# Kernel tuning notes

Hardware: AMD Instinct MI355X
Metric: run time of the kernel (lower is better)

## Reference

```python
import jax, jax.numpy as jnp
import numpy as np

N = 50000      # nodes
E = 1600000    # edges (avg degree 32)
F_IN = 128
HID = 256
C = 40


def setup_inputs() -> dict:
    key = jax.random.key(0)
    ks = jax.random.split(key, 12)
    x = jax.random.normal(ks[0], (N, F_IN), jnp.float32)
    edge_index = jax.random.randint(ks[1], (2, E), 0, N, dtype=jnp.int32)

    def glorot(k, fan_in, fan_out):
        s = jnp.sqrt(2.0 / (fan_in + fan_out)).astype(jnp.float32)
        return jax.random.normal(k, (fan_in, fan_out), jnp.float32) * s

    return {
        "x": x,
        "edge_index": edge_index,
        "W1": glorot(ks[2], F_IN, HID), "b1": jnp.zeros((HID,), jnp.float32),
        "W2": glorot(ks[3], HID, HID),  "b2": jnp.zeros((HID,), jnp.float32),
        "W3": glorot(ks[4], HID, HID),  "b3": jnp.zeros((HID,), jnp.float32),
        "W4": glorot(ks[5], HID, C),    "b4": jnp.zeros((C,), jnp.float32),
    }


def _gcn_conv(x, W, b, src, dst, norm_e, self_norm):
    # PyG GCNConv: h = X W; out_j = sum_i norm_ij * h_i  (+ self-loop term) + b
    h = x @ W                                   # [N, F_out]
    msg = h[src] * norm_e[:, None]              # [E, F_out] gather + scale
    agg = jax.ops.segment_sum(msg, dst, num_segments=N)
    agg = agg + h * self_norm[:, None]          # self-loop contribution
    return agg + b


def reference(x, edge_index, W1, b1, W2, b2, W3, b3, W4, b4):
    src, dst = edge_index[0], edge_index[1]
    # degree on A + I (self-loops added), computed over destination nodes
    deg = jax.ops.segment_sum(jnp.ones((E,), x.dtype), dst, num_segments=N) + 1.0
    inv_sqrt = jax.lax.rsqrt(deg)               # [N]
    norm_e = inv_sqrt[src] * inv_sqrt[dst]      # [E] symmetric norm per edge
    self_norm = inv_sqrt * inv_sqrt             # [N] self-loop norm = 1/deg

    h = jax.nn.relu(_gcn_conv(x, W1, b1, src, dst, norm_e, self_norm))
    h = jax.nn.relu(_gcn_conv(h, W2, b2, src, dst, norm_e, self_norm))
    h = jax.nn.relu(_gcn_conv(h, W3, b3, src, dst, norm_e, self_norm))
    h = _gcn_conv(h, W4, b4, src, dst, norm_e, self_norm)
    return jax.nn.log_softmax(h, axis=1)
```

## Files before the change

kernel.cpp:

```cpp
#include <hip/hip_runtime.h>
#include <hip/hip_fp16.h>
#include <math.h>


typedef _Float16 f16x8 __attribute__((ext_vector_type(8)));
typedef float f32x4 __attribute__((ext_vector_type(4)));
typedef unsigned u32x4 __attribute__((ext_vector_type(4)));

#define CAP 80
#define EPB 8192
#define MAXHDW 25024

#define AS1 __attribute__((address_space(1)))
#define AS3 __attribute__((address_space(3)))

__device__ __forceinline__ void dma16(const unsigned short* g,
                                      const unsigned short* ldsBase) {
    __builtin_amdgcn_global_load_lds((const AS1 void*)(size_t)g,
                                     (AS3 void*)(unsigned)(size_t)ldsBase,
                                     16, 0, 0);
}

__device__ __forceinline__ __half2 u2h2(unsigned u) {
    union { unsigned u; __half2 h; } v; v.u = u; return v.h;
}
__device__ __forceinline__ unsigned h22u(__half2 h) {
    union { unsigned u; __half2 h; } v; v.h = h; return v.u;
}
__device__ __forceinline__ float hlo(unsigned u) {
    return __half2float(__ushort_as_half((unsigned short)(u & 0xFFFFu)));
}
__device__ __forceinline__ float hhi(unsigned u) {
    return __half2float(__ushort_as_half((unsigned short)(u >> 16)));
}

__global__ __launch_bounds__(256) void count_lds_kernel(
        const int* __restrict__ dst, unsigned* __restrict__ bcnt,
        int E, int HDW) {
    __shared__ unsigned hist[MAXHDW];
    for (int i = threadIdx.x; i < HDW; i += 256) hist[i] = 0;
    __syncthreads();
    int b = blockIdx.x;
    int end = (b + 1) * EPB; if (end > E) end = E;
    for (int e0 = b * EPB + threadIdx.x * 4; e0 < end; e0 += 1024) {
        if (e0 + 3 < end) {
            int4 d4 = *reinterpret_cast<const int4*>(dst + e0);
            atomicAdd(&hist[d4.x >> 1], 1u << ((d4.x & 1) * 16));
            atomicAdd(&hist[d4.y >> 1], 1u << ((d4.y & 1) * 16));
            atomicAdd(&hist[d4.z >> 1], 1u << ((d4.z & 1) * 16));
            atomicAdd(&hist[d4.w >> 1], 1u << ((d4.w & 1) * 16));
        } else {
            for (int e = e0; e < end && e < e0 + 4; e++) {
                int d = dst[e];
                atomicAdd(&hist[d >> 1], 1u << ((d & 1) * 16));
            }
        }
    }
    __syncthreads();
    unsigned* out = bcnt + (size_t)b * HDW;
    for (int i = threadIdx.x; i < HDW; i += 256) out[i] = hist[i];
}

__global__ __launch_bounds__(256) void scan_prep_kernel(
        unsigned* __restrict__ bcnt, int nb, int HDW,
        int* __restrict__ cnt, float* __restrict__ rsq, int N, int scanBlocks,
        const float* __restrict__ x, unsigned short* __restrict__ xb, int nx4,
        const float* __restrict__ W1, const float* __restrict__ W2,
        const float* __restrict__ W3, const float* __restrict__ W4,
        unsigned short* __restrict__ Wt1, unsigned short* __restrict__ Wt2,
        unsigned short* __restrict__ Wt3, unsigned short* __restrict__ Wt4) {
    int blk = blockIdx.x;
    if (blk < scanBlocks) {
        int i = blk * 256 + threadIdx.x;
        if (i >= HDW) return;
        unsigned* bc = bcnt + i;
        unsigned acc0 = 0, acc1 = 0;
        int b = 0;
        for (; b + 3 < nb; b += 4) {
            unsigned w0 = bc[(size_t)(b + 0) * HDW];
            unsigned w1 = bc[(size_t)(b + 1) * HDW];
            unsigned w2 = bc[(size_t)(b + 2) * HDW];
            unsigned w3 = bc[(size_t)(b + 3) * HDW];
            bc[(size_t)(b + 0) * HDW] = acc0 | (acc1 << 16);
            acc0 += w0 & 0xFFFFu; acc1 += w0 >> 16;
            bc[(size_t)(b + 1) * HDW] = acc0 | (acc1 << 16);
            acc0 += w1 & 0xFFFFu; acc1 += w1 >> 16;
            bc[(size_t)(b + 2) * HDW] = acc0 | (acc1 << 16);
            acc0 += w2 & 0xFFFFu; acc1 += w2 >> 16;
            bc[(size_t)(b + 3) * HDW] = acc0 | (acc1 << 16);
            acc0 += w3 & 0xFFFFu; acc1 += w3 >> 16;
        }
        for (; b < nb; b++) {
            unsigned w = bc[(size_t)b * HDW];
            bc[(size_t)b * HDW] = acc0 | (acc1 << 16);
            acc0 += w & 0xFFFFu; acc1 += w >> 16;
        }
        int n0 = 2 * i, n1 = 2 * i + 1;
        if (n0 < N) {
            cnt[n0] = (int)acc0;
            rsq[n0] = rsqrtf((float)acc0 + 1.0f);
        }
        if (n1 < N) {
            cnt[n1] = (int)acc1;
            rsq[n1] = rsqrtf((float)acc1 + 1.0f);
        }
        return;
    }
    int i = (blk - scanBlocks) * 256 + threadIdx.x;
    if (i < nx4) {
        float4 v = reinterpret_cast<const float4*>(x)[i];
        ushort4 o;
        o.x = __half_as_ushort(__float2half_rn(v.x));
        o.y = __half_as_ushort(__float2half_rn(v.y));
        o.z = __half_as_ushort(__float2half_rn(v.z));
        o.w = __half_as_ushort(__float2half_rn(v.w));
        reinterpret_cast<ushort4*>(xb)[i] = o;
        return;
    }
    int j = i - nx4;
    if (j < 32768) {
        int k = j >> 8, n = j & 255;
        Wt1[n * 128 + k] = __half_as_ushort(__float2half_rn(W1[j]));
    } else if (j < 98304) {
        int t = j - 32768; int k = t >> 8, n = t & 255;
        Wt2[n * 256 + k] = __half_as_ushort(__float2half_rn(W2[t]));
    } else if (j < 163840) {
        int t = j - 98304; int k = t >> 8, n = t & 255;
        Wt3[n * 256 + k] = __half_as_ushort(__float2half_rn(W3[t]));
    } else if (j < 174080) {
        int t = j - 163840; int k = t / 40, n = t - k * 40;
        Wt4[n * 256 + k] = __half_as_ushort(__float2half_rn(W4[t]));
    }
}

__global__ __launch_bounds__(256) void scatter_lds_kernel(
        const int* __restrict__ src, const int* __restrict__ dst,
        const unsigned* __restrict__ bcnt, unsigned short* __restrict__ epk,
        int E, int HDW) {
    __shared__ unsigned hist[MAXHDW];
    int b = blockIdx.x;
    const unsigned* base = bcnt + (size_t)b * HDW;
    for (int i = threadIdx.x; i < HDW; i += 256) hist[i] = base[i];
    __syncthreads();
    int end = (b + 1) * EPB; if (end > E) end = E;
    for (int e0 = b * EPB + threadIdx.x * 4; e0 < end; e0 += 1024) {
        if (e0 + 3 < end) {
            int4 s4 = *reinterpret_cast<const int4*>(src + e0);
            int4 d4 = *reinterpret_cast<const int4*>(dst + e0);
            int dd[4] = {d4.x, d4.y, d4.z, d4.w};
            int ss[4] = {s4.x, s4.y, s4.z, s4.w};
            #pragma unroll
            for (int j = 0; j < 4; j++) {
                int d = dd[j];
                unsigned old = atomicAdd(&hist[d >> 1], 1u << ((d & 1) * 16));
                int slot = (int)((old >> ((d & 1) * 16)) & 0xFFFFu);
                if (slot >= CAP) slot = CAP - 1;
                epk[(size_t)d * CAP + slot] = (unsigned short)ss[j];
            }
        } else {
            for (int e = e0; e < end && e < e0 + 4; e++) {
                int d = dst[e];
                unsigned old = atomicAdd(&hist[d >> 1], 1u << ((d & 1) * 16));
                int slot = (int)((old >> ((d & 1) * 16)) & 0xFFFFu);
                if (slot >= CAP) slot = CAP - 1;
                epk[(size_t)d * CAP + slot] = (unsigned short)src[e];
            }
        }
    }
}

template <int ROWB, bool WSRC, bool BIAS, bool RELU>
__global__ __launch_bounds__(256) void agg_wide_kernel(
        const unsigned short* __restrict__ G,
        const int* __restrict__ cnt,
        const unsigned short* __restrict__ epk,
        const float* __restrict__ rsq,
        const float* __restrict__ bias,
        unsigned short* __restrict__ out, int N) {
    constexpr int ROWS = ROWB / 2;
    constexpr int LPN = ROWB / 16;
    constexpr int LOG_LPN = (LPN == 32) ? 5 : 4;
    constexpr int NPW = 64 / LPN;
    int lane = threadIdx.x & 63;
    int wid = threadIdx.x >> 6;
    int sub = lane >> LOG_LPN;
    int off = lane & (LPN - 1);
    int node = blockIdx.x * (4 * NPW) + wid * NPW + sub;
    if (node >= N) return;

    const unsigned short* gb = G + off * 8;
    const unsigned short* ep = epk + (size_t)node * CAP;
    int deg = cnt[node]; if (deg > CAP) deg = CAP;

    __half2 acc[4];
    #pragma unroll
    for (int k = 0; k < 4; k++) acc[k] = u2h2(0u);

    int e = 0;
    for (; e + 7 < deg; e += 8) {
        uint4 pv = *reinterpret_cast<const uint4*>(ep + e);
        int s[8];
        s[0] = pv.x & 0xFFFFu; s[1] = pv.x >> 16;
        s[2] = pv.y & 0xFFFFu; s[3] = pv.y >> 16;
        s[4] = pv.z & 0xFFFFu; s[5] = pv.z >> 16;
        s[6] = pv.w & 0xFFFFu; s[7] = pv.w >> 16;
        uint4 v[8];
        #pragma unroll
        for (int j = 0; j < 8; j++)
            v[j] = *reinterpret_cast<const uint4*>(gb + (size_t)s[j] * ROWS);
        if (WSRC) {
            float ws[8];
            #pragma unroll
            for (int j = 0; j < 8; j++) ws[j] = rsq[s[j]];
            #pragma unroll
            for (int j = 0; j < 8; j++) {
                __half2 w2 = __half2half2(__float2half_rn(ws[j]));
                acc[0] = __hfma2(w2, u2h2(v[j].x), acc[0]);
                acc[1] = __hfma2(w2, u2h2(v[j].y), acc[1]);
                acc[2] = __hfma2(w2, u2h2(v[j].z), acc[2]);
                acc[3] = __hfma2(w2, u2h2(v[j].w), acc[3]);
            }
        } else {
            #pragma unroll
            for (int j = 0; j < 8; j++) {
                acc[0] = __hadd2(acc[0], u2h2(v[j].x));
                acc[1] = __hadd2(acc[1], u2h2(v[j].y));
                acc[2] = __hadd2(acc[2], u2h2(v[j].z));
                acc[3] = __hadd2(acc[3], u2h2(v[j].w));
            }
        }
    }
    for (; e < deg; e++) {
        int s0 = ep[e];
        uint4 v0 = *reinterpret_cast<const uint4*>(gb + (size_t)s0 * ROWS);
        if (WSRC) {
            __half2 w2 = __half2half2(__float2half_rn(rsq[s0]));
            acc[0] = __hfma2(w2, u2h2(v0.x), acc[0]);
            acc[1] = __hfma2(w2, u2h2(v0.y), acc[1]);
            acc[2] = __hfma2(w2, u2h2(v0.z), acc[2]);
            acc[3] = __hfma2(w2, u2h2(v0.w), acc[3]);
        } else {
            acc[0] = __hadd2(acc[0], u2h2(v0.x));
            acc[1] = __hadd2(acc[1], u2h2(v0.y));
            acc[2] = __hadd2(acc[2], u2h2(v0.z));
            acc[3] = __hadd2(acc[3], u2h2(v0.w));
        }
    }

    float r = rsq[node];
    uint4 sv = *reinterpret_cast<const uint4*>(gb + (size_t)node * ROWS);
    unsigned svu[4] = {sv.x, sv.y, sv.z, sv.w};
    float sw = WSRC ? r : 1.0f;
    float r2 = r * r;
    u32x4 wp;
    float4 bv0, bv1;
    if (!WSRC && BIAS) {
        bv0 = reinterpret_cast<const float4*>(bias)[off * 2];
        bv1 = reinterpret_cast<const float4*>(bias)[off * 2 + 1];
    }
    float bvf[8] = {bv0.x, bv0.y, bv0.z, bv0.w, bv1.x, bv1.y, bv1.z, bv1.w};
    #pragma unroll
    for (int k = 0; k < 4; k++) {
        float2 f = __half22float2(acc[k]);
        f.x = fmaf(sw, hlo(svu[k]), f.x);
        f.y = fmaf(sw, hhi(svu[k]), f.y);
        float ox, oy;
        if (WSRC) {
            ox = r * f.x; oy = r * f.y;
        } else {
            ox = r2 * f.x; oy = r2 * f.y;
            if (BIAS) {
                ox = fmaf(r, bvf[2 * k], ox);
                oy = fmaf(r, bvf[2 * k + 1], oy);
            }
            if (RELU) { ox = fmaxf(ox, 0.f); oy = fmaxf(oy, 0.f); }
        }
        wp[k] = h22u(__floats2half2_rn(ox, oy));
    }
    __builtin_nontemporal_store(
        wp, reinterpret_cast<u32x4*>(out + (size_t)node * ROWS + off * 8));
}

__global__ __launch_bounds__(256) void agg40_softmax_kernel(
        const unsigned short* __restrict__ G,
        const int* __restrict__ cnt,
        const unsigned short* __restrict__ epk,
        const float* __restrict__ rsq,
        const float* __restrict__ bias,
        float* __restrict__ out, int N) {
    __shared__ __align__(16) unsigned red[4][64][4];
    int lane = threadIdx.x & 63;
    int wid = threadIdx.x >> 6;
    int node = blockIdx.x * 4 + wid;
    if (node >= N) return;
    const unsigned short* ep = epk + (size_t)node * CAP;
    int deg = cnt[node]; if (deg > CAP) deg = CAP;

    int j = lane / 5;
    int c = lane - j * 5;
    __half2 a0 = u2h2(0u), a1 = u2h2(0u), a2 = u2h2(0u), a3 = u2h2(0u);
    for (int e0 = 0; e0 < deg; e0 += 12) {
        int e = e0 + j;
        unsigned m = (j < 12 && e < deg) ? 0xFFFFFFFFu : 0u;
        int ee = (e < deg) ? e : (deg - 1);
        int s = ep[ee];
        u32x4 v = *reinterpret_cast<const u32x4*>(G + (size_t)s * 64 + c * 8);
        a0 = __hadd2(a0, u2h2(v.x & m));
        a1 = __hadd2(a1, u2h2(v.y & m));
        a2 = __hadd2(a2, u2h2(v.z & m));
        a3 = __hadd2(a3, u2h2(v.w & m));
    }
    u32x4 packed;
    packed.x = h22u(a0); packed.y = h22u(a1);
    packed.z = h22u(a2); packed.w = h22u(a3);
    *reinterpret_cast<u32x4*>(&red[wid][lane][0]) = packed;
    bool act = lane < 20;
    __half2 acch = u2h2(0u);
    if (act) {
        int cc = lane >> 2;
        int w = lane & 3;
        #pragma unroll
        for (int jj = 0; jj < 12; jj++)
            acch = __hadd2(acch, u2h2(red[wid][5 * jj + cc][w]));
    }
    float lo = 0.f, hi = 0.f;
    if (act) {
        float r = rsq[node];
        unsigned sv = reinterpret_cast<const unsigned*>(G)[(size_t)node * 32 + lane];
        float2 f = __half22float2(acch);
        f.x += hlo(sv); f.y += hhi(sv);
        lo = fmaf(r, f.x, bias[2 * lane]);
        hi = fmaf(r, f.y, bias[2 * lane + 1]);
    }
    float m = act ? fmaxf(lo, hi) : -INFINITY;
    #pragma unroll
    for (int o = 32; o >= 1; o >>= 1) m = fmaxf(m, __shfl_xor(m, o, 64));
    float s = act ? (expf(lo - m) + expf(hi - m)) : 0.f;
    #pragma unroll
    for (int o = 32; o >= 1; o >>= 1) s += __shfl_xor(s, o, 64);
    float ls = logf(s);
    if (act) {
        float2 o2;
        o2.x = lo - m - ls;
        o2.y = hi - m - ls;
        *reinterpret_cast<float2*>(out + (size_t)node * 40 + 2 * lane) = o2;
    }
}

template <int BK, bool BIAS, bool RELU, bool SCALE>
__global__ __launch_bounds__(256) void gemm_f16(
        const unsigned short* __restrict__ A,
        const unsigned short* __restrict__ Bt,
        const float* __restrict__ bias,
        const float* __restrict__ rsqRow,
        unsigned short* __restrict__ Cout,
        int M, int K, int Nc, int ldc) {
    constexpr int SPR = BK / 8;
    constexpr int NSTG = (128 * SPR) / 256;
    __shared__ __align__(16) unsigned short As[128 * BK];
    __shared__ __align__(16) unsigned short Bs[128 * BK];
    int tid = threadIdx.x;
    int lane = tid & 63;
    int wid = tid >> 6;
    int rowBase = blockIdx.y * 128;
    int colBase = blockIdx.x * 128;
    int waveM = (wid & 1) * 64;
    int waveN = (wid >> 1) * 64;

    f32x4 acc[4][4] = {};
    int lrow = lane & 15;
    int kgrp = (lane >> 4) * 8;

    for (int k0 = 0; k0 < K; k0 += BK) {
        #pragma unroll
        for (int c = 0; c < NSTG; c++) {
            int base16 = c * 256 + wid * 64;
            int slot = base16 + lane;
            int row = slot / SPR;
            int kp = (slot % SPR) * 8;
            int ksw = kp ^ ((row & (SPR - 1)) * 8);
            int gr = rowBase + row; if (gr >= M) gr = M - 1;
            dma16(A + (size_t)gr * K + k0 + ksw, &As[base16 * 8]);
            int gc = colBase + row; if (gc >= Nc) gc = Nc - 1;
            dma16(Bt + (size_t)gc * K + k0 + ksw, &Bs[base16 * 8]);
        }
        __syncthreads();
        #pragma unroll
        for (int kk = 0; kk < BK; kk += 32) {
            f16x8 af[4], bfr[4];
            #pragma unroll
            for (int t = 0; t < 4; t++) {
                int ra = waveM + t * 16 + lrow;
                af[t] = *reinterpret_cast<const f16x8*>(
                    &As[ra * BK + ((kk + kgrp) ^ ((ra & (SPR - 1)) * 8))]);
                int rb = waveN + t * 16 + lrow;
                bfr[t] = *reinterpret_cast<const f16x8*>(
                    &Bs[rb * BK + ((kk + kgrp) ^ ((rb & (SPR - 1)) * 8))]);
            }
            #pragma unroll
            for (int mt = 0; mt < 4; mt++)
                #pragma unroll
                for (int nt = 0; nt < 4; nt++)
                    acc[mt][nt] = __builtin_amdgcn_mfma_f32_16x16x32_f16(
                        af[mt], bfr[nt], acc[mt][nt], 0, 0, 0);
        }
        __syncthreads();
    }

    #pragma unroll
    for (int mt = 0; mt < 4; mt++) {
        #pragma unroll
        for (int r = 0; r < 4; r++) {
            int row = rowBase + waveM + mt * 16 + (lane >> 4) * 4 + r;
            if (row >= M) continue;
            float rs = SCALE ? rsqRow[row] : 1.0f;
            #pragma unroll
            for (int nt = 0; nt < 4; nt++) {
                int col = colBase + waveN + nt * 16 + (lane & 15);
                if (col >= Nc) continue;
                float v = acc[mt][nt][r];
                if (BIAS) v += bias[col];
                if (RELU) v = fmaxf(v, 0.f);
                if (SCALE) v *= rs;
                Cout[(size_t)row * ldc + col] = __half_as_ushort(__float2half_rn(v));
            }
        }
    }
}


extern "C" void kernel_launch(void* const* d_in, const int* in_sizes, int n_in,
                              void* d_out, int out_size, void* d_ws, size_t ws_size,
                              hipStream_t stream) {
    const float* x  = (const float*)d_in[0];
    const int*   ei = (const int*)d_in[1];
    const float* W1 = (const float*)d_in[2];
    const float* b1 = (const float*)d_in[3];
    const float* W2 = (const float*)d_in[4];
    const float* b2 = (const float*)d_in[5];
    const float* W3 = (const float*)d_in[6];
    const float* b3 = (const float*)d_in[7];
    const float* W4 = (const float*)d_in[8];
    const float* b4 = (const float*)d_in[9];

    const int FIN = 128, HID = 256, C = 40;
    const int N = in_sizes[0] / FIN;
    const int E = in_sizes[1] / 2;
    const int* src = ei;
    const int* dst = ei + E;
    const int HDW = (N + 1) / 2;
    const int nb = (E + EPB - 1) / EPB;

    char* w = (char*)d_ws;
    auto alloc = [&](size_t bytes) {
        char* p = w;
        w += (bytes + 255) & ~(size_t)255;
        return p;
    };
    int*   cnt    = (int*)alloc((size_t)N * 4);
    float* rsq    = (float*)alloc((size_t)N * 4);
    unsigned* bcnt = (unsigned*)alloc((size_t)nb * HDW * 4);
    unsigned short* epk = (unsigned short*)alloc((size_t)N * CAP * 2);
    unsigned short* aggx = (unsigned short*)alloc((size_t)N * FIN * 2);
    unsigned short* bufA = (unsigned short*)alloc((size_t)N * HID * 2);
    unsigned short* bufB = (unsigned short*)alloc((size_t)N * HID * 2);
    unsigned short* Wt1 = (unsigned short*)alloc((size_t)FIN * HID * 2);
    unsigned short* Wt2 = (unsigned short*)alloc((size_t)HID * HID * 2);
    unsigned short* Wt3 = (unsigned short*)alloc((size_t)HID * HID * 2);
    unsigned short* Wt4 = (unsigned short*)alloc((size_t)HID * C * 2);
    unsigned short* xb = bufB;

    int nx4 = N * FIN / 4;
    int scanBlocks = (HDW + 255) / 256;
    int prepBlocks = (nx4 + 174080 + 255) / 256;

    count_lds_kernel<<<nb, 256, 0, stream>>>(dst, bcnt, E, HDW);
    scan_prep_kernel<<<scanBlocks + prepBlocks, 256, 0, stream>>>(
        bcnt, nb, HDW, cnt, rsq, N, scanBlocks,
        x, xb, nx4, W1, W2, W3, W4, Wt1, Wt2, Wt3, Wt4);
    scatter_lds_kernel<<<nb, 256, 0, stream>>>(src, dst, bcnt, epk, E, HDW);

    dim3 gAgg1((N + 15) / 16);
    dim3 gAggH((N + 7) / 8);
    int grp = (N + 3) / 4;
    dim3 gHID((HID + 127) / 128, (N + 127) / 128);
    dim3 gC((C + 127) / 128, (N + 127) / 128);

    agg_wide_kernel<256, true, false, false>
        <<<gAgg1, 256, 0, stream>>>(xb, cnt, epk, rsq, nullptr, aggx, N);
    gemm_f16<128, true, true, true><<<gHID, 256, 0, stream>>>(
        aggx, Wt1, b1, rsq, bufA, N, FIN, HID, HID);
    gemm_f16<128, false, false, false><<<gHID, 256, 0, stream>>>(
        bufA, Wt2, nullptr, nullptr, bufB, N, HID, HID, HID);
    agg_wide_kernel<512, false, true, true>
        <<<gAggH, 256, 0, stream>>>(bufB, cnt, epk, rsq, b2, bufA, N);
    gemm_f16<128, false, false, false><<<gHID, 256, 0, stream>>>(
        bufA, Wt3, nullptr, nullptr, bufB, N, HID, HID, HID);
    agg_wide_kernel<512, false, true, true>
        <<<gAggH, 256, 0, stream>>>(bufB, cnt, epk, rsq, b3, bufA, N);
    gemm_f16<128, false, false, false><<<gC, 256, 0, stream>>>(
        bufA, Wt4, nullptr, nullptr, bufB, N, HID, C, 64);
    agg40_softmax_kernel<<<grp, 256, 0, stream>>>(bufB, cnt, epk,
                                                  rsq, b4, (float*)d_out, N);
}
```

Baseline: 525.6 us.

## Compute all output column tiles per block to reuse the A tile

```diff
diff --git a/kernel.cpp b/kernel.cpp
--- a/kernel.cpp
+++ b/kernel.cpp
@@ -347,7 +347,7 @@
     }
 }
 
-template <int BK, bool BIAS, bool RELU, bool SCALE>
+template <int BK, int NCT, bool BIAS, bool RELU, bool SCALE>
 __global__ __launch_bounds__(256) void gemm_f16(
         const unsigned short* __restrict__ A,
         const unsigned short* __restrict__ Bt,
@@ -363,11 +363,10 @@
     int lane = tid & 63;
     int wid = tid >> 6;
     int rowBase = blockIdx.y * 128;
-    int colBase = blockIdx.x * 128;
     int waveM = (wid & 1) * 64;
     int waveN = (wid >> 1) * 64;
 
-    f32x4 acc[4][4] = {};
+    f32x4 acc[NCT][4][4] = {};
     int lrow = lane & 15;
     int kgrp = (lane >> 4) * 8;
 
@@ -381,48 +380,63 @@
             int ksw = kp ^ ((row & (SPR - 1)) * 8);
             int gr = rowBase + row; if (gr >= M) gr = M - 1;
             dma16(A + (size_t)gr * K + k0 + ksw, &As[base16 * 8]);
-            int gc = colBase + row; if (gc >= Nc) gc = Nc - 1;
-            dma16(Bt + (size_t)gc * K + k0 + ksw, &Bs[base16 * 8]);
-        }
-        __syncthreads();
+        }
         #pragma unroll
-        for (int kk = 0; kk < BK; kk += 32) {
-            f16x8 af[4], bfr[4];
-            #pragma unroll
-            for (int t = 0; t < 4; t++) {
-                int ra = waveM + t * 16 + lrow;
-                af[t] = *reinterpret_cast<const f16x8*>(
-                    &As[ra * BK + ((kk + kgrp) ^ ((ra & (SPR - 1)) * 8))]);
-                int rb = waveN + t * 16 + lrow;
-                bfr[t] = *reinterpret_cast<const f16x8*>(
-                    &Bs[rb * BK + ((kk + kgrp) ^ ((rb & (SPR - 1)) * 8))]);
-            }
-            #pragma unroll
-            for (int mt = 0; mt < 4; mt++)
+        for (int ct = 0; ct < NCT; ct++) {
+            #pragma unroll
+            for (int c = 0; c < NSTG; c++) {
+                int base16 = c * 256 + wid * 64;
+                int slot = base16 + lane;
+                int row = slot / SPR;
+                int kp = (slot % SPR) * 8;
+                int ksw = kp ^ ((row & (SPR - 1)) * 8);
+                int gc = ct * 128 + row; if (gc >= Nc) gc = Nc - 1;
+                dma16(Bt + (size_t)gc * K + k0 + ksw, &Bs[base16 * 8]);
+            }
+            __syncthreads();
+            #pragma unroll
+            for (int kk = 0; kk < BK; kk += 32) {
+                f16x8 af[4], bfr[4];
                 #pragma unroll
-                for (int nt = 0; nt < 4; nt++)
-                    acc[mt][nt] = __builtin_amdgcn_mfma_f32_16x16x32_f16(
-                        af[mt], bfr[nt], acc[mt][nt], 0, 0, 0);
-        }
-        __syncthreads();
+                for (int t = 0; t < 4; t++) {
+                    int ra = waveM + t * 16 + lrow;
+                    af[t] = *reinterpret_cast<const f16x8*>(
+                        &As[ra * BK + ((kk + kgrp) ^ ((ra & (SPR - 1)) * 8))]);
+                    int rb = waveN + t * 16 + lrow;
+                    bfr[t] = *reinterpret_cast<const f16x8*>(
+                        &Bs[rb * BK + ((kk + kgrp) ^ ((rb & (SPR - 1)) * 8))]);
+                }
+                #pragma unroll
+                for (int mt = 0; mt < 4; mt++)
+                    #pragma unroll
+                    for (int nt = 0; nt < 4; nt++)
+                        acc[ct][mt][nt] = __builtin_amdgcn_mfma_f32_16x16x32_f16(
+                            af[mt], bfr[nt], acc[ct][mt][nt], 0, 0, 0);
+            }
+            __syncthreads();
+        }
     }
 
     #pragma unroll
-    for (int mt = 0; mt < 4; mt++) {
+    for (int ct = 0; ct < NCT; ct++) {
         #pragma unroll
-        for (int r = 0; r < 4; r++) {
-            int row = rowBase + waveM + mt * 16 + (lane >> 4) * 4 + r;
-            if (row >= M) continue;
-            float rs = SCALE ? rsqRow[row] : 1.0f;
-            #pragma unroll
-            for (int nt = 0; nt < 4; nt++) {
-                int col = colBase + waveN + nt * 16 + (lane & 15);
-                if (col >= Nc) continue;
-                float v = acc[mt][nt][r];
-                if (BIAS) v += bias[col];
-                if (RELU) v = fmaxf(v, 0.f);
-                if (SCALE) v *= rs;
-                Cout[(size_t)row * ldc + col] = __half_as_ushort(__float2half_rn(v));
+        for (int mt = 0; mt < 4; mt++) {
+            #pragma unroll
+            for (int r = 0; r < 4; r++) {
+                int row = rowBase + waveM + mt * 16 + (lane >> 4) * 4 + r;
+                if (row >= M) continue;
+                float rs = SCALE ? rsqRow[row] : 1.0f;
+                #pragma unroll
+                for (int nt = 0; nt < 4; nt++) {
+                    int col = ct * 128 + waveN + nt * 16 + (lane & 15);
+                    if (col >= Nc) continue;
+                    float v = acc[ct][mt][nt][r];
+                    if (BIAS) v += bias[col];
+                    if (RELU) v = fmaxf(v, 0.f);
+                    if (SCALE) v *= rs;
+                    Cout[(size_t)row * ldc + col] =
+                        __half_as_ushort(__float2half_rn(v));
+                }
             }
         }
     }
@@ -483,22 +497,21 @@
     dim3 gAgg1((N + 15) / 16);
     dim3 gAggH((N + 7) / 8);
     int grp = (N + 3) / 4;
-    dim3 gHID((HID + 127) / 128, (N + 127) / 128);
-    dim3 gC((C + 127) / 128, (N + 127) / 128);
+    dim3 gRows(1, (N + 127) / 128);
 
     agg_wide_kernel<256, true, false, false>
         <<<gAgg1, 256, 0, stream>>>(xb, cnt, epk, rsq, nullptr, aggx, N);
-    gemm_f16<128, true, true, true><<<gHID, 256, 0, stream>>>(
+    gemm_f16<128, 2, true, true, true><<<gRows, 256, 0, stream>>>(
         aggx, Wt1, b1, rsq, bufA, N, FIN, HID, HID);
-    gemm_f16<128, false, false, false><<<gHID, 256, 0, stream>>>(
+    gemm_f16<128, 2, false, false, false><<<gRows, 256, 0, stream>>>(
         bufA, Wt2, nullptr, nullptr, bufB, N, HID, HID, HID);
     agg_wide_kernel<512, false, true, true>
         <<<gAggH, 256, 0, stream>>>(bufB, cnt, epk, rsq, b2, bufA, N);
-    gemm_f16<128, false, false, false><<<gHID, 256, 0, stream>>>(
+    gemm_f16<128, 2, false, false, false><<<gRows, 256, 0, stream>>>(
         bufA, Wt3, nullptr, nullptr, bufB, N, HID, HID, HID);
     agg_wide_kernel<512, false, true, true>
         <<<gAggH, 256, 0, stream>>>(bufB, cnt, epk, rsq, b3, bufA, N);
-    gemm_f16<128, false, false, false><<<gC, 256, 0, stream>>>(
+    gemm_f16<128, 1, false, false, false><<<gRows, 256, 0, stream>>>(
         bufA, Wt4, nullptr, nullptr, bufB, N, HID, C, 64);
     agg40_softmax_kernel<<<grp, 256, 0, stream>>>(bufB, cnt, epk,
                                                   rsq, b4, (float*)d_out, N);
```

After: 554.9 us. +5.6%, slower.
